# Performance work log

Measured on AMD Instinct MI355X. Metric: run time of the kernel, lower is better.

The kernel has to match this reference:

```python
import jax, jax.numpy as jnp
import numpy as np
import math

N, D = 8192, 64
KSIZE = 1.0


def setup_inputs() -> dict:
    key = jax.random.key(0)
    kx, kz = jax.random.split(key)
    X = jax.random.normal(kx, (N, D), dtype=jnp.float32)
    Z = jax.random.normal(kz, (N, D), dtype=jnp.float32)
    return {"X": X, "Z": Z}


def _kernel_mean(A, B, ksize):
    # squared pairwise distances via the Gram-matrix expansion instead of
    # materializing the [N, M, D] broadcast diff the torch code implies.
    a2 = jnp.sum(A * A, axis=-1)                      # [N]
    b2 = jnp.sum(B * B, axis=-1)                      # [M]
    d2 = a2[:, None] + b2[None, :] - 2.0 * (A @ B.T)  # [N, M]
    d2 = jnp.maximum(d2, 0.0)                         # numerical guard
    G = jnp.exp(-d2 / ksize) / math.sqrt(2.0 * math.pi * ksize)
    return jnp.mean(G)


def reference(X, Z):
    mxx = _kernel_mean(X, X, KSIZE)
    mzz = _kernel_mean(Z, Z, KSIZE)
    mxz = _kernel_mean(X, Z, KSIZE)
    return jnp.log(jnp.sqrt(mxx * mzz + 1e-5) / (mxz + 1e-5))
```

## Files before the change

kernel.cpp:

```cpp
#include <hip/hip_runtime.h>
#include <hip/hip_bf16.h>
#include <math.h>

#define NN 8192
#define DD 64
#define TILES_SYM 2080
#define T2B (2*TILES_SYM)
#define TILES_TOTAL 8256
#define TILES_PER_BLOCK 8
#define NBLOCKS (TILES_TOTAL / TILES_PER_BLOCK)
#define NSLOT 32
#define SLOT_STRIDE 16

#define PANEL_ELEMS 1024

typedef __bf16 bf16x8 __attribute__((ext_vector_type(8)));
typedef float f32x4 __attribute__((ext_vector_type(4)));

#if defined(__has_builtin)
#if __has_builtin(__builtin_amdgcn_exp2f)
#define EXP2F __builtin_amdgcn_exp2f
#endif
#endif
#ifndef EXP2F
#define EXP2F exp2f
#endif


__global__ __launch_bounds__(256) void prep_kernel(
        const float* __restrict__ X, const float* __restrict__ Z,
        __hip_bfloat16* __restrict__ XbF, __hip_bfloat16* __restrict__ ZbF,
        float* __restrict__ na, float* __restrict__ nb,
        float* __restrict__ partial) {
    int tid = threadIdx.x;
    int gw = blockIdx.x * 4 + (tid >> 6);
    int lane = tid & 63;
    int lm = lane & 15, lk = lane >> 4;
    const float* src = (gw < 512) ? X : Z;
    __hip_bfloat16* dst = (gw < 512) ? XbF : ZbF;
    float* nrm = (gw < 512) ? na : nb;
    int p = (gw < 512) ? gw : gw - 512;
    int row = p * 16 + lm;

    float s = 0.f;
    #pragma unroll
    for (int ks = 0; ks < 2; ++ks) {
        const float4* q = (const float4*)(src + (size_t)row * DD + ks * 32 + lk * 8);
        float4 u = q[0], v = q[1];
        float w[8] = {u.x, u.y, u.z, u.w, v.x, v.y, v.z, v.w};
        unsigned int h[8];
        #pragma unroll
        for (int r = 0; r < 8; ++r) {
            __hip_bfloat16 b = __float2bfloat16(w[r]);
            h[r] = *(unsigned short*)&b;
            float xr = __bfloat162float(b);
            s = fmaf(xr, xr, s);
        }
        uint4 pk;
        pk.x = h[0] | (h[1] << 16); pk.y = h[2] | (h[3] << 16);
        pk.z = h[4] | (h[5] << 16); pk.w = h[6] | (h[7] << 16);
        *(uint4*)(dst + (size_t)p * PANEL_ELEMS + ks * 512 + lane * 8) = pk;
    }
    s += __shfl_xor(s, 16, 64);
    s += __shfl_xor(s, 32, 64);
    if (lk == 0) nrm[row] = -1.4426950408889634f * s;

    if (blockIdx.x == 0) {
        for (int i = tid; i < 3 * NSLOT * SLOT_STRIDE; i += 256) partial[i] = 0.f;
    }
}

__global__ __launch_bounds__(256) void mmd_kernel(
        const __hip_bfloat16* __restrict__ XbFh, const __hip_bfloat16* __restrict__ ZbFh,
        const float* __restrict__ na, const float* __restrict__ nb,
        float* __restrict__ partial) {
    int tid = threadIdx.x;
    int wave = tid >> 6, lane = tid & 63;
    int wr = wave >> 1, wc = wave & 1;
    int lm = lane & 15;
    int lk = lane >> 4;
    __shared__ float wsum[4];
    const float C2 = 2.8853900817779268f;

    int t0 = blockIdx.x * TILES_PER_BLOCK;
    int combo, bi, bj;
    if (t0 < T2B) {
        combo = (t0 < TILES_SYM) ? 0 : 1;
        int tt = (t0 < TILES_SYM) ? t0 : t0 - TILES_SYM;
        int rr = (int)((129.0f - sqrtf(16641.0f - 8.0f * (float)tt)) * 0.5f);
        if (rr < 0) rr = 0;
        while (rr > 0 && rr * (129 - rr) / 2 > tt) --rr;
        while ((rr + 1) * (128 - rr) / 2 <= tt) ++rr;
        bi = rr;
        bj = rr + (tt - rr * (129 - rr) / 2);
    } else {
        combo = 2;
        int rem = t0 - T2B;
        bi = rem >> 6;
        bj = rem & 63;
    }
    const bool sym = (combo != 2);
    const __bf16 *A, *B;
    const float *sa, *sb;
    const __bf16* XbF = (const __bf16*)XbFh;
    const __bf16* ZbF = (const __bf16*)ZbFh;
    if (combo == 0)      { A = XbF; B = XbF; sa = na; sb = na; }
    else if (combo == 1) { A = ZbF; B = ZbF; sa = nb; sb = nb; }
    else                 { A = XbF; B = ZbF; sa = na; sb = nb; }

    bf16x8 af[2][4];
    float nav[4][4], navrtmax[4], navmax;
    {
        int pA = bi * 8 + wr * 4;
        #pragma unroll
        for (int ks = 0; ks < 2; ++ks)
            #pragma unroll
            for (int rt = 0; rt < 4; ++rt)
                af[ks][rt] = *(const bf16x8*)(A + (size_t)(pA + rt) * PANEL_ELEMS + ks * 512 + lane * 8);
        int row0 = bi * 128 + wr * 64;
        #pragma unroll
        for (int rt = 0; rt < 4; ++rt) {
            #pragma unroll
            for (int r = 0; r < 4; ++r) nav[rt][r] = sa[row0 + rt * 16 + lk * 4 + r];
            navrtmax[rt] = fmaxf(fmaxf(nav[rt][0], nav[rt][1]), fmaxf(nav[rt][2], nav[rt][3]));
        }
        navmax = fmaxf(fmaxf(navrtmax[0], navrtmax[1]), fmaxf(navrtmax[2], navrtmax[3]));
    }

    bf16x8 bufB[2][2][4];
    float bufNb[2][4];
    {
        int pB = bj * 8 + wc * 4;
        #pragma unroll
        for (int ks = 0; ks < 2; ++ks)
            #pragma unroll
            for (int ct = 0; ct < 4; ++ct)
                bufB[0][ks][ct] = *(const bf16x8*)(B + (size_t)(pB + ct) * PANEL_ELEMS + ks * 512 + lane * 8);
        int col0 = bj * 128 + wc * 64;
        #pragma unroll
        for (int ct = 0; ct < 4; ++ct) bufNb[0][ct] = sb[col0 + ct * 16 + lm];
    }

    float lsum = 0.f;

    #pragma unroll
    for (int it = 0; it < TILES_PER_BLOCK; ++it) {
        const int cur = it & 1, nxt = cur ^ 1;
        const bool last = (it + 1 == TILES_PER_BLOCK);
        bool diag = sym && (bi == bj);
        float tileScale = (sym && bj > bi) ? 2.f : 1.f;
        int row0 = bi * 128 + wr * 64;
        int col0 = bj * 128 + wc * 64;

        int nbi = bi, nbj = bj;
        if (!last) {
            nbj = bj + 1;
            if (nbj == 64) { nbi = bi + 1; nbj = sym ? nbi : 0; }
            int npB = nbj * 8 + wc * 4;
            #pragma unroll
            for (int ks = 0; ks < 2; ++ks)
                #pragma unroll
                for (int ct = 0; ct < 4; ++ct)
                    bufB[nxt][ks][ct] = *(const bf16x8*)(B + (size_t)(npB + ct) * PANEL_ELEMS + ks * 512 + lane * 8);
            int ncol0 = nbj * 128 + wc * 64;
            #pragma unroll
            for (int ct = 0; ct < 4; ++ct) bufNb[nxt][ct] = sb[ncol0 + ct * 16 + lm];
        }
        __builtin_amdgcn_sched_barrier(0);

        f32x4 acc[4][4] = {};
        #pragma unroll
        for (int ks = 0; ks < 2; ++ks)
            #pragma unroll
            for (int rt = 0; rt < 4; ++rt)
                #pragma unroll
                for (int ct = 0; ct < 4; ++ct)
                    acc[rt][ct] = __builtin_amdgcn_mfma_f32_16x16x32_bf16(
                        af[ks][rt], bufB[cur][ks][ct], acc[rt][ct], 0, 0, 0);

        float gmax = fmaxf(fmaxf(acc[0][0][0], acc[0][0][1]), fmaxf(acc[0][0][2], acc[0][0][3]));
        #pragma unroll
        for (int rt = 0; rt < 4; ++rt)
            #pragma unroll
            for (int ct = 0; ct < 4; ++ct)
                if (rt || ct) {
                    float m = fmaxf(fmaxf(acc[rt][ct][0], acc[rt][ct][1]),
                                    fmaxf(acc[rt][ct][2], acc[rt][ct][3]));
                    gmax = fmaxf(gmax, m);
                }
        float nbmax = fmaxf(fmaxf(bufNb[cur][0], bufNb[cur][1]), fmaxf(bufNb[cur][2], bufNb[cur][3]));
        float tileBound = fmaf(gmax, C2, navmax + nbmax);
        if (__any(tileBound > -30.f)) {
            #pragma unroll
            for (int rt = 0; rt < 4; ++rt) {
                #pragma unroll
                for (int ct = 0; ct < 4; ++ct) {
                    float fm = fmaxf(fmaxf(acc[rt][ct][0], acc[rt][ct][1]),
                                     fmaxf(acc[rt][ct][2], acc[rt][ct][3]));
                    float fb = fmaf(fm, C2, navrtmax[rt] + bufNb[cur][ct]);
                    if (__any(fb > -30.f)) {
                        float base = bufNb[cur][ct];
                        float a0 = fmaf(acc[rt][ct][0], C2, nav[rt][0] + base);
                        float a1 = fmaf(acc[rt][ct][1], C2, nav[rt][1] + base);
                        float a2 = fmaf(acc[rt][ct][2], C2, nav[rt][2] + base);
                        float a3 = fmaf(acc[rt][ct][3], C2, nav[rt][3] + base);
                        float e0 = EXP2F(fminf(a0, 0.f));
                        float e1 = EXP2F(fminf(a1, 0.f));
                        float e2 = EXP2F(fminf(a2, 0.f));
                        float e3 = EXP2F(fminf(a3, 0.f));
                        if (diag) {
                            int gcol = col0 + ct * 16 + lm;
                            int gr = row0 + rt * 16 + lk * 4;
                            e0 *= (gr + 0 < gcol) ? 2.f : ((gr + 0 == gcol) ? 1.f : 0.f);
                            e1 *= (gr + 1 < gcol) ? 2.f : ((gr + 1 == gcol) ? 1.f : 0.f);
                            e2 *= (gr + 2 < gcol) ? 2.f : ((gr + 2 == gcol) ? 1.f : 0.f);
                            e3 *= (gr + 3 < gcol) ? 2.f : ((gr + 3 == gcol) ? 1.f : 0.f);
                            lsum += (e0 + e1) + (e2 + e3);
                        } else {
                            lsum += tileScale * ((e0 + e1) + (e2 + e3));
                        }
                    }
                }
            }
        }

        if (!last && nbi != bi) {
            int npA = nbi * 8 + wr * 4;
            #pragma unroll
            for (int ks = 0; ks < 2; ++ks)
                #pragma unroll
                for (int rt = 0; rt < 4; ++rt)
                    af[ks][rt] = *(const bf16x8*)(A + (size_t)(npA + rt) * PANEL_ELEMS + ks * 512 + lane * 8);
            int nrow0 = nbi * 128 + wr * 64;
            #pragma unroll
            for (int rt = 0; rt < 4; ++rt) {
                #pragma unroll
                for (int r = 0; r < 4; ++r) nav[rt][r] = sa[nrow0 + rt * 16 + lk * 4 + r];
                navrtmax[rt] = fmaxf(fmaxf(nav[rt][0], nav[rt][1]), fmaxf(nav[rt][2], nav[rt][3]));
            }
            navmax = fmaxf(fmaxf(navrtmax[0], navrtmax[1]), fmaxf(navrtmax[2], navrtmax[3]));
            __builtin_amdgcn_sched_barrier(0);
        }
        bi = nbi; bj = nbj;
    }

    #pragma unroll
    for (int off = 32; off; off >>= 1) lsum += __shfl_xor(lsum, off, 64);
    if (lane == 0) wsum[wave] = lsum;
    __syncthreads();
    if (tid == 0) {
        float s = (wsum[0] + wsum[1]) + (wsum[2] + wsum[3]);
        int slot = combo * NSLOT + (blockIdx.x & (NSLOT - 1));
        atomicAdd(&partial[slot * SLOT_STRIDE], s);
    }
}

__global__ void final_kernel(const float* __restrict__ partial, float* __restrict__ out) {
    __shared__ float s3[3];
    int tid = threadIdx.x;
    if (tid < 3) s3[tid] = 0.f;
    __syncthreads();
    if (tid < 3 * NSLOT) {
        float v = partial[tid * SLOT_STRIDE];
        atomicAdd(&s3[tid / NSLOT], v);
    }
    __syncthreads();
    if (tid == 0) {
        double inv = 1.0 / ((double)NN * (double)NN * 2.5066282746310002);
        double mxx = (double)s3[0] * inv;
        double mzz = (double)s3[1] * inv;
        double mxz = (double)s3[2] * inv;
        double v = log(sqrt(mxx * mzz + 1e-5) / (mxz + 1e-5));
        out[0] = (float)v;
    }
}

extern "C" void kernel_launch(void* const* d_in, const int* in_sizes, int n_in,
                              void* d_out, int out_size, void* d_ws, size_t ws_size,
                              hipStream_t stream) {
    const float* X = (const float*)d_in[0];
    const float* Z = (const float*)d_in[1];
    char* ws = (char*)d_ws;
    __hip_bfloat16* XbF = (__hip_bfloat16*)(ws);
    __hip_bfloat16* ZbF = (__hip_bfloat16*)(ws + 1048576);
    float* na = (float*)(ws + 2097152);
    float* nb = (float*)(ws + 2097152 + 32768);
    float* partial = (float*)(ws + 2097152 + 65536);

    hipLaunchKernelGGL(prep_kernel, dim3(256), dim3(256), 0, stream,
                       X, Z, XbF, ZbF, na, nb, partial);
    hipLaunchKernelGGL(mmd_kernel, dim3(NBLOCKS), dim3(256), 0, stream, XbF, ZbF, na, nb, partial);
    hipLaunchKernelGGL(final_kernel, dim3(1), dim3(128), 0, stream, partial, (float*)d_out);
}
```

Baseline: 35.13 us.

## Stage B panels through LDS with direct global-to-LDS loads shared by waves

Replaces the per-wave register prefetch of B fragments with global_load_lds staging into a double-buffered LDS tile. Each wave now loads a quarter of the B panel instead of two waves redundantly loading the same columns, and MFMAs read B fragments from LDS. This cuts duplicate global traffic and register pressure, but adds a block-wide barrier every tile and LDS read latency. No explicit wait on the async LDS loads beyond __syncthreads is visible, so correctness relies on the barrier draining vmcnt.

Result: slower. 39.41 us (+12.2%).

```diff
diff --git a/kernel.cpp b/kernel.cpp
--- a/kernel.cpp
+++ b/kernel.cpp
@@ -13,6 +13,7 @@
 #define SLOT_STRIDE 16
 
 #define PANEL_ELEMS 1024
+#define LDS_TILE 16384
 
 typedef __bf16 bf16x8 __attribute__((ext_vector_type(8)));
 typedef float f32x4 __attribute__((ext_vector_type(4)));
@@ -80,6 +81,7 @@
     int lm = lane & 15;
     int lk = lane >> 4;
     __shared__ float wsum[4];
+    __shared__ char ldsB[2][LDS_TILE];
     const float C2 = 2.8853900817779268f;
 
     int t0 = blockIdx.x * TILES_PER_BLOCK;
@@ -127,15 +129,27 @@
         navmax = fmaxf(fmaxf(navrtmax[0], navrtmax[1]), fmaxf(navrtmax[2], navrtmax[3]));
     }
 
-    bf16x8 bufB[2][2][4];
+#define STAGE_B(BUFI, BJ)                                                            \
+    {                                                                                \
+        int pl0 = wave * 2;                                                          \
+        _Pragma("unroll")                                                            \
+        for (int pl2 = 0; pl2 < 2; ++pl2) {                                          \
+            _Pragma("unroll")                                                        \
+            for (int ks = 0; ks < 2; ++ks) {                                         \
+                const __bf16* gsrc = B + (size_t)((BJ) * 8 + pl0 + pl2) * PANEL_ELEMS \
+                                       + ks * 512 + lane * 8;                        \
+                __builtin_amdgcn_global_load_lds(                                    \
+                    (const __attribute__((address_space(1))) void*)gsrc,             \
+                    (__attribute__((address_space(3))) void*)                        \
+                        (&ldsB[BUFI][(pl0 + pl2) * 2048 + ks * 1024]),               \
+                    16, 0, 0);                                                       \
+            }                                                                        \
+        }                                                                            \
+    }
+
+    STAGE_B(0, bj)
     float bufNb[2][4];
     {
-        int pB = bj * 8 + wc * 4;
-        #pragma unroll
-        for (int ks = 0; ks < 2; ++ks)
-            #pragma unroll
-            for (int ct = 0; ct < 4; ++ct)
-                bufB[0][ks][ct] = *(const bf16x8*)(B + (size_t)(pB + ct) * PANEL_ELEMS + ks * 512 + lane * 8);
         int col0 = bj * 128 + wc * 64;
         #pragma unroll
         for (int ct = 0; ct < 4; ++ct) bufNb[0][ct] = sb[col0 + ct * 16 + lm];
@@ -152,16 +166,13 @@
         int row0 = bi * 128 + wr * 64;
         int col0 = bj * 128 + wc * 64;
 
+        __syncthreads();
+
         int nbi = bi, nbj = bj;
         if (!last) {
             nbj = bj + 1;
             if (nbj == 64) { nbi = bi + 1; nbj = sym ? nbi : 0; }
-            int npB = nbj * 8 + wc * 4;
-            #pragma unroll
-            for (int ks = 0; ks < 2; ++ks)
-                #pragma unroll
-                for (int ct = 0; ct < 4; ++ct)
-                    bufB[nxt][ks][ct] = *(const bf16x8*)(B + (size_t)(npB + ct) * PANEL_ELEMS + ks * 512 + lane * 8);
+            STAGE_B(nxt, nbj)
             int ncol0 = nbj * 128 + wc * 64;
             #pragma unroll
             for (int ct = 0; ct < 4; ++ct) bufNb[nxt][ct] = sb[ncol0 + ct * 16 + lm];
@@ -170,13 +181,18 @@
 
         f32x4 acc[4][4] = {};
         #pragma unroll
-        for (int ks = 0; ks < 2; ++ks)
+        for (int ks = 0; ks < 2; ++ks) {
+            bf16x8 bfr[4];
+            #pragma unroll
+            for (int ct = 0; ct < 4; ++ct)
+                bfr[ct] = *(const bf16x8*)(&ldsB[cur][(wc * 4 + ct) * 2048 + ks * 1024 + lane * 16]);
             #pragma unroll
             for (int rt = 0; rt < 4; ++rt)
                 #pragma unroll
                 for (int ct = 0; ct < 4; ++ct)
                     acc[rt][ct] = __builtin_amdgcn_mfma_f32_16x16x32_bf16(
-                        af[ks][rt], bufB[cur][ks][ct], acc[rt][ct], 0, 0, 0);
+                        af[ks][rt], bfr[ct], acc[rt][ct], 0, 0, 0);
+        }
 
         float gmax = fmaxf(fmaxf(acc[0][0][0], acc[0][0][1]), fmaxf(acc[0][0][2], acc[0][0][3]));
         #pragma unroll
@@ -243,6 +259,7 @@
         }
         bi = nbi; bj = nbj;
     }
+#undef STAGE_B
 
     #pragma unroll
     for (int off = 32; off; off >>= 1) lsum += __shfl_xor(lsum, off, 64);
```

## Shrink tile columns to 64 and double tiles per block

Applied to the files above, without the earlier changes.

Changes the tile shape from 128x128 to 128x64 (each wave computes 64x32), doubling the tile count and tiles per block while keeping the block count. The upper-triangular tile enumeration is rederived for the rectangular tiling, and diagonal masking becomes a per-wave element-wise check. The aim is finer-grained triangular coverage, so less work is wasted on diagonal tiles, plus finer early-exit skipping. The cost is less reuse of the A fragments per B load and more loop overhead.

After: 34.50 us. About the same (-1.8%).

```diff
diff --git a/kernel.cpp b/kernel.cpp
--- a/kernel.cpp
+++ b/kernel.cpp
@@ -4,11 +4,14 @@
 
 #define NN 8192
 #define DD 64
-#define TILES_SYM 2080
-#define T2B (2*TILES_SYM)
-#define TILES_TOTAL 8256
-#define TILES_PER_BLOCK 8
-#define NBLOCKS (TILES_TOTAL / TILES_PER_BLOCK)
+#define BI_MAX 64
+#define BJ_MAX 128
+#define TRI_N 4160
+#define T1B TRI_N
+#define T2B (2*TRI_N)
+#define TILES_TOTAL 16512
+#define TPB 16
+#define NBLOCKS (TILES_TOTAL / TPB)
 #define NSLOT 32
 #define SLOT_STRIDE 16
 
@@ -82,22 +85,22 @@
     __shared__ float wsum[4];
     const float C2 = 2.8853900817779268f;
 
-    int t0 = blockIdx.x * TILES_PER_BLOCK;
+    int t0 = blockIdx.x * TPB;
     int combo, bi, bj;
     if (t0 < T2B) {
-        combo = (t0 < TILES_SYM) ? 0 : 1;
-        int tt = (t0 < TILES_SYM) ? t0 : t0 - TILES_SYM;
-        int rr = (int)((129.0f - sqrtf(16641.0f - 8.0f * (float)tt)) * 0.5f);
-        if (rr < 0) rr = 0;
-        while (rr > 0 && rr * (129 - rr) / 2 > tt) --rr;
-        while ((rr + 1) * (128 - rr) / 2 <= tt) ++rr;
+        combo = (t0 < T1B) ? 0 : 1;
+        int tt = t0 - (combo ? T1B : 0);
+        int rr = (int)((129.0f - sqrtf(16641.0f - 4.0f * (float)tt)) * 0.5f);
+        rr = rr < 0 ? 0 : (rr > 63 ? 63 : rr);
+        while (rr > 0 && rr * (129 - rr) > tt) --rr;
+        while ((rr + 1) * (128 - rr) <= tt) ++rr;
         bi = rr;
-        bj = rr + (tt - rr * (129 - rr) / 2);
+        bj = 2 * rr + (tt - rr * (129 - rr));
     } else {
         combo = 2;
         int rem = t0 - T2B;
-        bi = rem >> 6;
-        bj = rem & 63;
+        bi = rem >> 7;
+        bj = rem & 127;
     }
     const bool sym = (combo != 2);
     const __bf16 *A, *B;
@@ -127,54 +130,55 @@
         navmax = fmaxf(fmaxf(navrtmax[0], navrtmax[1]), fmaxf(navrtmax[2], navrtmax[3]));
     }
 
-    bf16x8 bufB[2][2][4];
-    float bufNb[2][4];
+    bf16x8 bufB[2][2][2];
+    float bufNb[2][2];
     {
-        int pB = bj * 8 + wc * 4;
+        int pB = bj * 4 + wc * 2;
         #pragma unroll
         for (int ks = 0; ks < 2; ++ks)
             #pragma unroll
-            for (int ct = 0; ct < 4; ++ct)
+            for (int ct = 0; ct < 2; ++ct)
                 bufB[0][ks][ct] = *(const bf16x8*)(B + (size_t)(pB + ct) * PANEL_ELEMS + ks * 512 + lane * 8);
-        int col0 = bj * 128 + wc * 64;
-        #pragma unroll
-        for (int ct = 0; ct < 4; ++ct) bufNb[0][ct] = sb[col0 + ct * 16 + lm];
+        int col0 = bj * 64 + wc * 32;
+        #pragma unroll
+        for (int ct = 0; ct < 2; ++ct) bufNb[0][ct] = sb[col0 + ct * 16 + lm];
     }
 
     float lsum = 0.f;
 
     #pragma unroll
-    for (int it = 0; it < TILES_PER_BLOCK; ++it) {
+    for (int it = 0; it < TPB; ++it) {
         const int cur = it & 1, nxt = cur ^ 1;
-        const bool last = (it + 1 == TILES_PER_BLOCK);
-        bool diag = sym && (bi == bj);
-        float tileScale = (sym && bj > bi) ? 2.f : 1.f;
+        const bool last = (it + 1 == TPB);
         int row0 = bi * 128 + wr * 64;
-        int col0 = bj * 128 + wc * 64;
+        int col0 = bj * 64 + wc * 32;
+        bool above = sym && (col0 >= row0 + 64);
+        bool elemw = sym && !above;
+        float tileScale = above ? 2.f : 1.f;
 
         int nbi = bi, nbj = bj;
         if (!last) {
             nbj = bj + 1;
-            if (nbj == 64) { nbi = bi + 1; nbj = sym ? nbi : 0; }
-            int npB = nbj * 8 + wc * 4;
+            if (nbj == BJ_MAX) { nbi = bi + 1; nbj = sym ? 2 * nbi : 0; }
+            int npB = nbj * 4 + wc * 2;
             #pragma unroll
             for (int ks = 0; ks < 2; ++ks)
                 #pragma unroll
-                for (int ct = 0; ct < 4; ++ct)
+                for (int ct = 0; ct < 2; ++ct)
                     bufB[nxt][ks][ct] = *(const bf16x8*)(B + (size_t)(npB + ct) * PANEL_ELEMS + ks * 512 + lane * 8);
-            int ncol0 = nbj * 128 + wc * 64;
-            #pragma unroll
-            for (int ct = 0; ct < 4; ++ct) bufNb[nxt][ct] = sb[ncol0 + ct * 16 + lm];
+            int ncol0 = nbj * 64 + wc * 32;
+            #pragma unroll
+            for (int ct = 0; ct < 2; ++ct) bufNb[nxt][ct] = sb[ncol0 + ct * 16 + lm];
         }
         __builtin_amdgcn_sched_barrier(0);
 
-        f32x4 acc[4][4] = {};
+        f32x4 acc[4][2] = {};
         #pragma unroll
         for (int ks = 0; ks < 2; ++ks)
             #pragma unroll
             for (int rt = 0; rt < 4; ++rt)
                 #pragma unroll
-                for (int ct = 0; ct < 4; ++ct)
+                for (int ct = 0; ct < 2; ++ct)
                     acc[rt][ct] = __builtin_amdgcn_mfma_f32_16x16x32_bf16(
                         af[ks][rt], bufB[cur][ks][ct], acc[rt][ct], 0, 0, 0);
 
@@ -182,19 +186,19 @@
         #pragma unroll
         for (int rt = 0; rt < 4; ++rt)
             #pragma unroll
-            for (int ct = 0; ct < 4; ++ct)
+            for (int ct = 0; ct < 2; ++ct)
                 if (rt || ct) {
                     float m = fmaxf(fmaxf(acc[rt][ct][0], acc[rt][ct][1]),
                                     fmaxf(acc[rt][ct][2], acc[rt][ct][3]));
                     gmax = fmaxf(gmax, m);
                 }
-        float nbmax = fmaxf(fmaxf(bufNb[cur][0], bufNb[cur][1]), fmaxf(bufNb[cur][2], bufNb[cur][3]));
+        float nbmax = fmaxf(bufNb[cur][0], bufNb[cur][1]);
         float tileBound = fmaf(gmax, C2, navmax + nbmax);
         if (__any(tileBound > -30.f)) {
             #pragma unroll
             for (int rt = 0; rt < 4; ++rt) {
                 #pragma unroll
-                for (int ct = 0; ct < 4; ++ct) {
+                for (int ct = 0; ct < 2; ++ct) {
                     float fm = fmaxf(fmaxf(acc[rt][ct][0], acc[rt][ct][1]),
                                      fmaxf(acc[rt][ct][2], acc[rt][ct][3]));
                     float fb = fmaf(fm, C2, navrtmax[rt] + bufNb[cur][ct]);
@@ -208,7 +212,7 @@
                         float e1 = EXP2F(fminf(a1, 0.f));
                         float e2 = EXP2F(fminf(a2, 0.f));
                         float e3 = EXP2F(fminf(a3, 0.f));
-                        if (diag) {
+                        if (elemw) {
                             int gcol = col0 + ct * 16 + lm;
                             int gr = row0 + rt * 16 + lk * 4;
                             e0 *= (gr + 0 < gcol) ? 2.f : ((gr + 0 == gcol) ? 1.f : 0.f);
```
